# Kernel optimization log

Hardware: AMD Instinct MI355X
Metric: run time of the kernel (lower is better)

## Reference

```python
import jax, jax.numpy as jnp
import numpy as np

B, S, D = 2, 2048, 2048
H, HKV, HD = 32, 8, 64
G = H // HKV  # num_key_value_groups


def setup_inputs() -> dict:
    key = jax.random.key(0)
    ks = jax.random.split(key, 9)
    sc = 0.02
    return {
        "x": jax.random.normal(ks[0], (B, S, D), jnp.float32),
        "wq": jax.random.normal(ks[1], (H * HD, D), jnp.float32) * sc,
        "bq": jax.random.normal(ks[2], (H * HD,), jnp.float32) * sc,
        "wk": jax.random.normal(ks[3], (HKV * HD, D), jnp.float32) * sc,
        "bk": jax.random.normal(ks[4], (HKV * HD,), jnp.float32) * sc,
        "wv": jax.random.normal(ks[5], (HKV * HD, D), jnp.float32) * sc,
        "bv": jax.random.normal(ks[6], (HKV * HD,), jnp.float32) * sc,
        "wo": jax.random.normal(ks[7], (D, H * HD), jnp.float32) * sc,
        "bo": jax.random.normal(ks[8], (D,), jnp.float32) * sc,
    }


def reference(x, wq, bq, wk, bk, wv, bv, wo, bo):
    b, s, _ = x.shape
    # fused-QKV-style projections (nn.Linear: x @ W.T + b)
    q = (jnp.einsum("bsd,ed->bse", x, wq) + bq).reshape(b, s, H, HD)
    k = (jnp.einsum("bsd,ed->bse", x, wk) + bk).reshape(b, s, HKV, HD)
    v = (jnp.einsum("bsd,ed->bse", x, wv) + bv).reshape(b, s, HKV, HD)
    # (B, Hkv, G, S, hd): grouped query heads share a KV head — same math as
    # repeat_kv (expand+flatten) without materializing the expanded KV tensor
    q = q.transpose(0, 2, 1, 3).reshape(b, HKV, G, s, HD)
    k = k.transpose(0, 2, 1, 3)  # (B, Hkv, S, hd)
    v = v.transpose(0, 2, 1, 3)
    scale = 1.0 / jnp.sqrt(jnp.asarray(HD, x.dtype))
    scores = jnp.einsum("bkgqd,bktd->bkgqt", q, k) * scale  # (B,Hkv,G,S,S)
    causal = jnp.tril(jnp.ones((s, s), bool))
    scores = jnp.where(causal, scores, jnp.asarray(-jnp.inf, scores.dtype))
    probs = jax.nn.softmax(scores, axis=-1)
    o = jnp.einsum("bkgqt,bktd->bkgqd", probs, v)  # (B,Hkv,G,S,hd)
    o = o.reshape(b, H, s, HD).transpose(0, 2, 1, 3).reshape(b, s, H * HD)
    return jnp.einsum("bse,de->bsd", o, wo) + bo
```

## Files before the change

### kernel.cpp

```cpp
#include <hip/hip_runtime.h>
#include <hip/hip_bf16.h>
#include <cmath>

#define B_   2
#define S_   2048
#define D_   2048
#define H_   32
#define HKV_ 8
#define HD_  64

using bf16 = __hip_bfloat16;
typedef __bf16    bf16x8 __attribute__((ext_vector_type(8)));
typedef float     floatx4 __attribute__((ext_vector_type(4)));
typedef _Float16  half4 __attribute__((ext_vector_type(4)));
typedef _Float16  half8 __attribute__((ext_vector_type(8)));
typedef _Float16  half2v __attribute__((ext_vector_type(2)));

#if __has_builtin(__builtin_amdgcn_exp2f)
#define EXP2(x) __builtin_amdgcn_exp2f(x)
#else
#define EXP2(x) exp2f(x)
#endif

#define QSCALE 0.18033688011112042f

__device__ inline void async16(const void* g, void* l) {
  __builtin_amdgcn_global_load_lds(
      (const __attribute__((address_space(1))) void*)g,
      (__attribute__((address_space(3))) void*)l, 16, 0, 0);
}

__device__ inline half2v pkrtz(float a, float b) {
  return __builtin_bit_cast(half2v, __builtin_amdgcn_cvt_pkrtz(a, b));
}

#define MFMA32B(a, b, c) __builtin_amdgcn_mfma_f32_16x16x32_bf16((a), (b), (c), 0, 0, 0)
#define MFMA16H(a, b, c) __builtin_amdgcn_mfma_f32_16x16x16f16((a), (b), (c), 0, 0, 0)

__global__ void f2b_all(const float* __restrict__ x,  const float* __restrict__ wq,
                        const float* __restrict__ wk, const float* __restrict__ wv,
                        const float* __restrict__ wo,
                        bf16* __restrict__ xb,  bf16* __restrict__ wqb,
                        bf16* __restrict__ wkb, bf16* __restrict__ wvb,
                        bf16* __restrict__ wob) {
  const int i = blockIdx.x * blockDim.x + threadIdx.x;
  const float* src; bf16* dst; int off; float scale = 1.0f;
  if (i < 1048576)      { src = x;  dst = xb;  off = 0; }
  else if (i < 1572864) { src = wq; dst = wqb; off = 1048576; scale = QSCALE; }
  else if (i < 1703936) { src = wk; dst = wkb; off = 1572864; }
  else if (i < 1835008) { src = wv; dst = wvb; off = 1703936; }
  else                  { src = wo; dst = wob; off = 1835008; }
  const int j = i - off;
  float4 a  = ((const float4*)src)[2 * j];
  float4 b2 = ((const float4*)src)[2 * j + 1];
  alignas(16) bf16 t[8];
  t[0] = __float2bfloat16(a.x * scale);  t[1] = __float2bfloat16(a.y * scale);
  t[2] = __float2bfloat16(a.z * scale);  t[3] = __float2bfloat16(a.w * scale);
  t[4] = __float2bfloat16(b2.x * scale); t[5] = __float2bfloat16(b2.y * scale);
  t[6] = __float2bfloat16(b2.z * scale); t[7] = __float2bfloat16(b2.w * scale);
  ((uint4*)dst)[j] = *(const uint4*)t;
}

__device__ inline void gemm_body(const bf16* __restrict__ Ag, const bf16* __restrict__ Bg,
                                 const float* __restrict__ bias,
                                 float* __restrict__ C, int Ncol, int K, int bm, int colb,
                                 bf16* As, bf16* Bs) {
  const int tid  = threadIdx.x;
  const int wid  = tid >> 6, lane = tid & 63;
  const int lm   = lane & 15, quad = lane >> 4;
  const int wm   = (wid >> 1) * 64, wn = (wid & 1) * 64;

  floatx4 acc[4][4] = {};

  const int l0 = tid * 8;
  const int r0 = l0 >> 5, c0 = l0 & 31;
  const int r1 = r0 + 64;

  for (int k0 = 0; k0 < K; k0 += 32) {
    async16(Ag + (size_t)r0 * K + k0 + c0, &As[l0]);
    async16(Ag + (size_t)r1 * K + k0 + c0, &As[l0 + 2048]);
    async16(Bg + (size_t)r0 * K + k0 + c0, &Bs[l0]);
    async16(Bg + (size_t)r1 * K + k0 + c0, &Bs[l0 + 2048]);
    asm volatile("s_waitcnt vmcnt(0)" ::: "memory");
    __syncthreads();

    bf16x8 aF[4], bF[4];
#pragma unroll
    for (int mi = 0; mi < 4; ++mi)
      aF[mi] = *(const bf16x8*)&As[(wm + mi * 16 + lm) * 32 + quad * 8];
#pragma unroll
    for (int ni = 0; ni < 4; ++ni)
      bF[ni] = *(const bf16x8*)&Bs[(wn + ni * 16 + lm) * 32 + quad * 8];
#pragma unroll
    for (int mi = 0; mi < 4; ++mi)
#pragma unroll
      for (int ni = 0; ni < 4; ++ni)
        acc[mi][ni] = MFMA32B(bF[ni], aF[mi], acc[mi][ni]);
    __syncthreads();
  }

#pragma unroll
  for (int mi = 0; mi < 4; ++mi) {
    const int row = bm * 128 + wm + mi * 16 + lm;
#pragma unroll
    for (int ni = 0; ni < 4; ++ni) {
      const int col0 = colb + wn + ni * 16 + quad * 4;
      float4 bv4 = *(const float4*)&bias[col0];
      float4 o4;
      o4.x = acc[mi][ni][0] + bv4.x; o4.y = acc[mi][ni][1] + bv4.y;
      o4.z = acc[mi][ni][2] + bv4.z; o4.w = acc[mi][ni][3] + bv4.w;
      *(float4*)&C[(size_t)row * Ncol + col0] = o4;
    }
  }
}

__global__ __launch_bounds__(256, 2)
void gemm_o(const bf16* __restrict__ A, const bf16* __restrict__ Bm,
            const float* __restrict__ bias, float* __restrict__ C,
            int Ncol, int K) {
  __shared__ bf16 As[128 * 32];
  __shared__ bf16 Bs[128 * 32];
  const int bn = blockIdx.x, bm = blockIdx.y;
  gemm_body(A + (size_t)bm * 128 * K, Bm + (size_t)bn * 128 * K, bias,
            C, Ncol, K, bm, bn * 128, As, Bs);
}

__global__ __launch_bounds__(512, 2)
void gemm_qkv8(const bf16* __restrict__ xb, const bf16* __restrict__ Wcat,
               const float* __restrict__ bq, const float* __restrict__ bk,
               const float* __restrict__ bv,
               bf16* __restrict__ Qo, bf16* __restrict__ Ko,
               _Float16* __restrict__ VG) {
  constexpr int NT = D_ / 64;
  __shared__ bf16 L[65536];

  const int id = blockIdx.x;
  const int bn = id & 7;
  const int bm = id >> 3;

  const int tid = threadIdx.x;
  const int wid = tid >> 6, lane = tid & 63;
  const int lm = lane & 15, quad = lane >> 4;
  const int wm = wid >> 2, wn = wid & 3;

  const int cOff = (quad * 8) ^ (((lm >> 3) & 1) << 4);
  const bf16* LA0 = L + (wm * 64 + lm) * 32 + cOff;
  const bf16* LB0 = L + 8192 + (wn * 96 + lm) * 32 + cOff;

  const int r0 = tid >> 2;
  const int csrc = ((tid & 3) * 8) ^ (((tid >> 5) & 1) << 4);
  const bf16* Asrc = xb   + (size_t)(bm * 128 + r0) * D_ + csrc;
  const bf16* Bs0  = Wcat + (size_t)(bn * 384 + r0) * D_ + csrc;
  const bf16* Bs1  = Bs0 + (size_t)128 * D_;
  const bf16* Bs2  = Bs0 + (size_t)256 * D_;
  bf16* Ld = L + tid * 8;

  floatx4 acc[4][6] = {};

#define BARX() { asm volatile("" ::: "memory"); __builtin_amdgcn_s_barrier(); \
                 asm volatile("" ::: "memory"); }
#define LGKM0() asm volatile("s_waitcnt lgkmcnt(0)" ::: "memory")
#define STG_A(tt, hh, DB)  async16(Asrc + (tt) * 64 + (hh) * 32, (DB) + (hh) * 4096)
#define STG_B0(tt, hh, DB) async16(Bs0  + (tt) * 64 + (hh) * 32, (DB) + 8192 + (hh) * 12288)
#define STG_B1(tt, hh, DB) async16(Bs1  + (tt) * 64 + (hh) * 32, (DB) + 8192 + (hh) * 12288 + 4096)
#define STG_B2(tt, hh, DB) async16(Bs2  + (tt) * 64 + (hh) * 32, (DB) + 8192 + (hh) * 12288 + 8192)

  STG_A(0, 0, Ld); STG_B0(0, 0, Ld); STG_B1(0, 0, Ld); STG_B2(0, 0, Ld);
  STG_A(0, 1, Ld); STG_B0(0, 1, Ld); STG_B1(0, 1, Ld); STG_B2(0, 1, Ld);
  STG_A(1, 0, Ld + 32768); STG_B0(1, 0, Ld + 32768);
  STG_B1(1, 0, Ld + 32768); STG_B2(1, 0, Ld + 32768);
  asm volatile("s_waitcnt vmcnt(8)" ::: "memory");
  BARX();

  auto tile = [&](int t, const int BUF) __attribute__((always_inline)) {
    const bf16* LA = LA0 + BUF;
    const bf16* LB = LB0 + BUF;
    bf16* SD  = Ld + BUF;
    bf16* SDo = Ld + (BUF ^ 32768);
    const bool s1 = (t + 1) < NT, s2 = (t + 2) < NT;
    bf16x8 aF[4], bF[3];

#pragma unroll
    for (int i = 0; i < 4; ++i) aF[i] = *(const bf16x8*)(LA + i * 512);
#pragma unroll
    for (int i = 0; i < 3; ++i) bF[i] = *(const bf16x8*)(LB + i * 512);
    if (s1) { STG_A(t + 1, 1, SDo); STG_B0(t + 1, 1, SDo); }
    BARX(); LGKM0();
    __builtin_amdgcn_s_setprio(1);
#pragma unroll
    for (int mi = 0; mi < 4; ++mi)
#pragma unroll
      for (int ni = 0; ni < 3; ++ni)
        acc[mi][ni] = MFMA32B(bF[ni], aF[mi], acc[mi][ni]);
    __builtin_amdgcn_s_setprio(0);
    BARX();

#pragma unroll
    for (int i = 0; i < 3; ++i) bF[i] = *(const bf16x8*)(LB + (i + 3) * 512);
    if (s1) { STG_B1(t + 1, 1, SDo); STG_B2(t + 1, 1, SDo); }
    BARX(); LGKM0();
    __builtin_amdgcn_s_setprio(1);
#pragma unroll
    for (int mi = 0; mi < 4; ++mi)
#pragma unroll
      for (int ni = 0; ni < 3; ++ni)
        acc[mi][ni + 3] = MFMA32B(bF[ni], aF[mi], acc[mi][ni + 3]);
    __builtin_amdgcn_s_setprio(0);
    if (s1) { asm volatile("s_waitcnt vmcnt(8)" ::: "memory"); }
    else    { asm volatile("s_waitcnt vmcnt(0)" ::: "memory"); }
    BARX();

#pragma unroll
    for (int i = 0; i < 4; ++i) aF[i] = *(const bf16x8*)(LA + 4096 + i * 512);
#pragma unroll
    for (int i = 0; i < 3; ++i) bF[i] = *(const bf16x8*)(LB + 12288 + i * 512);
    if (s2) { STG_A(t + 2, 0, SD); STG_B0(t + 2, 0, SD); }
    BARX(); LGKM0();
    __builtin_amdgcn_s_setprio(1);
#pragma unroll
    for (int mi = 0; mi < 4; ++mi)
#pragma unroll
      for (int ni = 0; ni < 3; ++ni)
        acc[mi][ni] = MFMA32B(bF[ni], aF[mi], acc[mi][ni]);
    __builtin_amdgcn_s_setprio(0);
    BARX();

#pragma unroll
    for (int i = 0; i < 3; ++i) bF[i] = *(const bf16x8*)(LB + 12288 + (i + 3) * 512);
    if (s2) { STG_B1(t + 2, 0, SD); STG_B2(t + 2, 0, SD); }
    BARX(); LGKM0();
    __builtin_amdgcn_s_setprio(1);
#pragma unroll
    for (int mi = 0; mi < 4; ++mi)
#pragma unroll
      for (int ni = 0; ni < 3; ++ni)
        acc[mi][ni + 3] = MFMA32B(bF[ni], aF[mi], acc[mi][ni + 3]);
    __builtin_amdgcn_s_setprio(0);
    if (s2)      { asm volatile("s_waitcnt vmcnt(8)" ::: "memory"); }
    else if (s1) { asm volatile("s_waitcnt vmcnt(4)" ::: "memory"); }
    else         { asm volatile("s_waitcnt vmcnt(0)" ::: "memory"); }
    BARX();
  };

  for (int t = 0; t < NT; t += 2) { tile(t, 0); tile(t + 1, 32768); }

#undef BARX
#undef LGKM0
#undef STG_A
#undef STG_B0
#undef STG_B1
#undef STG_B2

#pragma unroll
  for (int mi = 0; mi < 4; ++mi) {
    const int row = bm * 128 + wm * 64 + mi * 16 + lm;
#pragma unroll
    for (int ni = 0; ni < 6; ++ni) {
      const int colf = bn * 384 + wn * 96 + ni * 16;
      const int col0 = colf + quad * 4;
      if (colf < 2048) {
        float4 bv4 = *(const float4*)&bq[col0];
        alignas(8) bf16 t4[4];
#pragma unroll
        for (int r = 0; r < 4; ++r)
          t4[r] = __float2bfloat16(acc[mi][ni][r] + ((const float*)&bv4)[r] * QSCALE);
        *(uint2*)&Qo[(size_t)row * (H_ * HD_) + col0] = *(const uint2*)t4;
      } else if (colf < 2560) {
        const int ck = col0 - 2048;
        float4 bv4 = *(const float4*)&bk[ck];
        alignas(8) bf16 t4[4];
#pragma unroll
        for (int r = 0; r < 4; ++r)
          t4[r] = __float2bfloat16(acc[mi][ni][r] + ((const float*)&bv4)[r]);
        *(uint2*)&Ko[(size_t)row * (HKV_ * HD_) + ck] = *(const uint2*)t4;
      } else {
        const int cv = col0 - 2560;
        const int kvh = cv >> 6, hd = cv & 63;
        const int nh = hd >> 4;
        const int bb = row >> 11, s2 = row & 2047;
        const int tl = s2 >> 6, kvin = s2 & 63;
        const int kc = kvin >> 4, qd = (kvin >> 2) & 3, j = kvin & 3;
        const size_t base = ((size_t)((bb * 8 + kvh) * 32 + tl) << 12) +
                            (size_t)(((kc * 2 + (nh >> 1)) * 4 + qd) * 128 +
                                     (nh & 1) * 4 + j);
        float4 bv4 = *(const float4*)&bv[cv];
#pragma unroll
        for (int r = 0; r < 4; ++r)
          VG[base + (size_t)(quad * 4 + r) * 8] =
              (_Float16)(acc[mi][ni][r] + ((const float*)&bv4)[r]);
      }
    }
  }
}

__global__ __launch_bounds__(256, 5)
void attn_kernel(const bf16* __restrict__ Q, const bf16* __restrict__ K,
                 const _Float16* __restrict__ VG, bf16* __restrict__ O) {
  const int tid = threadIdx.x;
  const int wid = tid >> 6, lane = tid & 63;
  const int lm = lane & 15, quad = lane >> 4;

  const int n   = blockIdx.y * 64 + blockIdx.x;
  const int x3  = n & 7, b1 = (n >> 3) & 1;
  const int pair = n >> 4;
  const int grp  = x3 * 2 + b1;
  const int b    = grp >> 3, kvh = grp & 7;
  const int head = kvh * 4 + wid;

  const int hi = 127 - pair, lo = pair;
  const int nt_hi = (hi >> 2) + 1;
  const int nt_lo = (lo >> 2) + 1;

  __shared__ bf16     Ks[2 * 64 * 64];
  __shared__ _Float16 Vs[2 * 64 * 64];

  const int tb[2] = {hi * 16, lo * 16};

  bf16x8 qf[2][2];
#pragma unroll
  for (int tt = 0; tt < 2; ++tt) {
    const size_t qg = ((size_t)(b * S_ + tb[tt] + lm)) * (H_ * HD_) + head * HD_;
#pragma unroll
    for (int kf = 0; kf < 2; ++kf)
      qf[tt][kf] = *(const bf16x8*)&Q[qg + kf * 32 + quad * 8];
  }

  half4 onesh;
#pragma unroll
  for (int j = 0; j < 4; ++j) onesh[j] = (_Float16)1.0f;

  floatx4 o_acc[2][4] = {};
  floatx4 lacc[2] = {};

  auto stage = [&](int t, int buf) {
    const int tr = tid >> 2;
    const int tc = (tid & 3) * 8;
#pragma unroll
    for (int c = 0; c < 2; ++c) {
      async16(&K[(size_t)(b * S_ + t * 64 + tr) * (HKV_ * HD_) + kvh * HD_ + c * 32 + tc],
              &Ks[buf * 4096 + c * 2048 + tid * 8]);
      async16(&VG[((size_t)(grp * 32 + t) << 12) + c * 2048 + tid * 8],
              &Vs[buf * 4096 + c * 2048 + tid * 8]);
    }
  };

  stage(0, 0);

  for (int t = 0; t < nt_hi; ++t) {
    const int cur = t & 1;
    asm volatile("s_waitcnt vmcnt(0)" ::: "memory");
    __syncthreads();
    if (t + 1 < nt_hi) stage(t + 1, cur ^ 1);

    const bf16*     Kb = &Ks[cur * 4096];
    const _Float16* Vb = &Vs[cur * 4096];
    const int t0 = t * 64;
    const int nact = (t < nt_lo) ? 2 : 1;

    int kcmax[2], kcross[2];
#pragma unroll
    for (int tt = 0; tt < 2; ++tt) {
      const int rel = tb[tt] + 15 - t0;
      kcmax[tt]  = (tt < nact) ? ((rel >> 4) >= 3 ? 4 : (rel >> 4) + 1) : 0;
      kcross[tt] = rel >> 4;
    }

    half4 ps[2] = {};

#pragma unroll
    for (int kc = 0; kc < 4; ++kc) {
      if (kc >= kcmax[0]) break;
      bf16x8 kb0 = *(const bf16x8*)&Kb[(kc * 16 + lm) * 32 + quad * 8];
      bf16x8 kb1 = *(const bf16x8*)&Kb[2048 + (kc * 16 + lm) * 32 + quad * 8];

      floatx4 sT[2];
      __builtin_amdgcn_s_setprio(1);
#pragma unroll
      for (int tt = 0; tt < 2; ++tt) {
        if (kc >= kcmax[tt]) continue;
        floatx4 s0 = {};
        s0 = MFMA32B(kb0, qf[tt][0], s0);
        sT[tt] = MFMA32B(kb1, qf[tt][1], s0);
      }
      __builtin_amdgcn_s_setprio(0);

      half8 v0 = *(const half8*)&Vb[(kc * 8 + quad) * 128 + lm * 8];
      half8 v1 = *(const half8*)&Vb[(kc * 8 + 4 + quad) * 128 + lm * 8];
      half4 v0l = __builtin_shufflevector(v0, v0, 0, 1, 2, 3);
      half4 v0h = __builtin_shufflevector(v0, v0, 4, 5, 6, 7);
      half4 v1l = __builtin_shufflevector(v1, v1, 0, 1, 2, 3);
      half4 v1h = __builtin_shufflevector(v1, v1, 4, 5, 6, 7);

      half4 pbk[2];
#pragma unroll
      for (int tt = 0; tt < 2; ++tt) {
        if (kc >= kcmax[tt]) continue;
        floatx4 s = sT[tt];
        if (kc == kcross[tt]) {
          const int qrel = tb[tt] + lm - t0;
#pragma unroll
          for (int r = 0; r < 4; ++r)
            if (kc * 16 + quad * 4 + r > qrel) s[r] = -__builtin_inff();
        }
        half2v c0 = pkrtz(EXP2(s[0]), EXP2(s[1]));
        half2v c1 = pkrtz(EXP2(s[2]), EXP2(s[3]));
        half4 pk = __builtin_shufflevector(c0, c1, 0, 1, 2, 3);
        pbk[tt] = pk;
        ps[tt] += pk;
      }

      __builtin_amdgcn_s_setprio(1);
#pragma unroll
      for (int tt = 0; tt < 2; ++tt) {
        if (kc >= kcmax[tt]) continue;
        o_acc[tt][0] = MFMA16H(v0l, pbk[tt], o_acc[tt][0]);
        o_acc[tt][1] = MFMA16H(v0h, pbk[tt], o_acc[tt][1]);
        o_acc[tt][2] = MFMA16H(v1l, pbk[tt], o_acc[tt][2]);
        o_acc[tt][3] = MFMA16H(v1h, pbk[tt], o_acc[tt][3]);
      }
      __builtin_amdgcn_s_setprio(0);
    }

#pragma unroll
    for (int tt = 0; tt < 2; ++tt)
      if (kcmax[tt]) lacc[tt] = MFMA16H(onesh, ps[tt], lacc[tt]);
  }

#pragma unroll
  for (int tt = 0; tt < 2; ++tt) {
    const float rl = 1.f / lacc[tt][0];
    const size_t rowg = (size_t)(b * S_ + tb[tt] + lm);
#pragma unroll
    for (int nh = 0; nh < 4; ++nh) {
      alignas(8) bf16 tmp[4];
#pragma unroll
      for (int r = 0; r < 4; ++r)
        tmp[r] = __float2bfloat16(o_acc[tt][nh][r] * rl);
      *(uint2*)&O[rowg * (H_ * HD_) + head * HD_ + nh * 16 + quad * 4] = *(uint2*)tmp;
    }
  }
}

extern "C" void kernel_launch(void* const* d_in, const int* in_sizes, int n_in,
                              void* d_out, int out_size, void* d_ws, size_t ws_size,
                              hipStream_t stream) {
  (void)in_sizes; (void)n_in; (void)out_size; (void)ws_size;
  const float* x  = (const float*)d_in[0];
  const float* wq = (const float*)d_in[1];
  const float* bq = (const float*)d_in[2];
  const float* wk = (const float*)d_in[3];
  const float* bk = (const float*)d_in[4];
  const float* wv = (const float*)d_in[5];
  const float* bv = (const float*)d_in[6];
  const float* wo = (const float*)d_in[7];
  const float* bo = (const float*)d_in[8];
  float* out = (float*)d_out;

  const int M = B_ * S_;
  const int E = H_ * HD_;
  const int EKV = HKV_ * HD_;

  char* ws = (char*)d_ws;
  size_t off = 0;
  auto alloc = [&](size_t bytes) {
    char* p = ws + off;
    off += (bytes + 255) & ~(size_t)255;
    return p;
  };
  bf16* xb   = (bf16*)alloc((size_t)M * D_ * 2);
  bf16* Wcat = (bf16*)alloc((size_t)(E + 2 * EKV) * D_ * 2);
  bf16* wob  = (bf16*)alloc((size_t)D_ * E * 2);
  bf16* Qb   = (bf16*)alloc((size_t)M * E * 2);
  bf16* Kb   = (bf16*)alloc((size_t)M * EKV * 2);
  _Float16* VG = (_Float16*)alloc((size_t)M * EKV * 2);
  bf16* Ob   = (bf16*)alloc((size_t)M * E * 2);

  bf16* wqb = Wcat;
  bf16* wkb = Wcat + (size_t)E * D_;
  bf16* wvb = Wcat + (size_t)(E + EKV) * D_;

  f2b_all<<<9216, 256, 0, stream>>>(x, wq, wk, wv, wo, xb, wqb, wkb, wvb, wob);

  gemm_qkv8<<<dim3(256), dim3(512), 0, stream>>>(xb, Wcat, bq, bk, bv,
                                                 Qb, Kb, VG);

  attn_kernel<<<dim3(64, 16), 256, 0, stream>>>(Qb, Kb, VG, Ob);

  gemm_o<<<dim3(D_ / 128, M / 128), 256, 0, stream>>>(Ob, wob, bo, out, D_, D_);
}
```

Baseline: 291.9 us.

## Replace output GEMM with pipelined 8-wave kernel; merge QKV half-steps

Replaces the simple single-buffered output-projection GEMM with a 512-thread kernel that uses a 128x256 tile, double-buffered async global-to-LDS loads with swizzled layout, and MFMA priority hints, so loads overlap with compute. The QKV GEMM inner step is also restructured: all six B fragments are loaded at once and the two half-phases (with their extra barriers) are merged into one. This cuts barrier and synchronisation overhead. In exchange it raises register pressure and issues all stage loads together, which could hurt occupancy or latency hiding.

```diff
diff --git a/kernel.cpp b/kernel.cpp
--- a/kernel.cpp
+++ b/kernel.cpp
@@ -36,6 +36,10 @@
 
 #define MFMA32B(a, b, c) __builtin_amdgcn_mfma_f32_16x16x32_bf16((a), (b), (c), 0, 0, 0)
 #define MFMA16H(a, b, c) __builtin_amdgcn_mfma_f32_16x16x16f16((a), (b), (c), 0, 0, 0)
+
+#define BARX() { asm volatile("" ::: "memory"); __builtin_amdgcn_s_barrier(); \
+                 asm volatile("" ::: "memory"); }
+#define LGKM0() asm volatile("s_waitcnt lgkmcnt(0)" ::: "memory")
 
 __global__ void f2b_all(const float* __restrict__ x,  const float* __restrict__ wq,
                         const float* __restrict__ wk, const float* __restrict__ wv,
@@ -61,70 +65,6 @@
   ((uint4*)dst)[j] = *(const uint4*)t;
 }
 
-__device__ inline void gemm_body(const bf16* __restrict__ Ag, const bf16* __restrict__ Bg,
-                                 const float* __restrict__ bias,
-                                 float* __restrict__ C, int Ncol, int K, int bm, int colb,
-                                 bf16* As, bf16* Bs) {
-  const int tid  = threadIdx.x;
-  const int wid  = tid >> 6, lane = tid & 63;
-  const int lm   = lane & 15, quad = lane >> 4;
-  const int wm   = (wid >> 1) * 64, wn = (wid & 1) * 64;
-
-  floatx4 acc[4][4] = {};
-
-  const int l0 = tid * 8;
-  const int r0 = l0 >> 5, c0 = l0 & 31;
-  const int r1 = r0 + 64;
-
-  for (int k0 = 0; k0 < K; k0 += 32) {
-    async16(Ag + (size_t)r0 * K + k0 + c0, &As[l0]);
-    async16(Ag + (size_t)r1 * K + k0 + c0, &As[l0 + 2048]);
-    async16(Bg + (size_t)r0 * K + k0 + c0, &Bs[l0]);
-    async16(Bg + (size_t)r1 * K + k0 + c0, &Bs[l0 + 2048]);
-    asm volatile("s_waitcnt vmcnt(0)" ::: "memory");
-    __syncthreads();
-
-    bf16x8 aF[4], bF[4];
-#pragma unroll
-    for (int mi = 0; mi < 4; ++mi)
-      aF[mi] = *(const bf16x8*)&As[(wm + mi * 16 + lm) * 32 + quad * 8];
-#pragma unroll
-    for (int ni = 0; ni < 4; ++ni)
-      bF[ni] = *(const bf16x8*)&Bs[(wn + ni * 16 + lm) * 32 + quad * 8];
-#pragma unroll
-    for (int mi = 0; mi < 4; ++mi)
-#pragma unroll
-      for (int ni = 0; ni < 4; ++ni)
-        acc[mi][ni] = MFMA32B(bF[ni], aF[mi], acc[mi][ni]);
-    __syncthreads();
-  }
-
-#pragma unroll
-  for (int mi = 0; mi < 4; ++mi) {
-    const int row = bm * 128 + wm + mi * 16 + lm;
-#pragma unroll
-    for (int ni = 0; ni < 4; ++ni) {
-      const int col0 = colb + wn + ni * 16 + quad * 4;
-      float4 bv4 = *(const float4*)&bias[col0];
-      float4 o4;
-      o4.x = acc[mi][ni][0] + bv4.x; o4.y = acc[mi][ni][1] + bv4.y;
-      o4.z = acc[mi][ni][2] + bv4.z; o4.w = acc[mi][ni][3] + bv4.w;
-      *(float4*)&C[(size_t)row * Ncol + col0] = o4;
-    }
-  }
-}
-
-__global__ __launch_bounds__(256, 2)
-void gemm_o(const bf16* __restrict__ A, const bf16* __restrict__ Bm,
-            const float* __restrict__ bias, float* __restrict__ C,
-            int Ncol, int K) {
-  __shared__ bf16 As[128 * 32];
-  __shared__ bf16 Bs[128 * 32];
-  const int bn = blockIdx.x, bm = blockIdx.y;
-  gemm_body(A + (size_t)bm * 128 * K, Bm + (size_t)bn * 128 * K, bias,
-            C, Ncol, K, bm, bn * 128, As, Bs);
-}
-
 __global__ __launch_bounds__(512, 2)
 void gemm_qkv8(const bf16* __restrict__ xb, const bf16* __restrict__ Wcat,
                const float* __restrict__ bq, const float* __restrict__ bk,
@@ -157,9 +97,6 @@
 
   floatx4 acc[4][6] = {};
 
-#define BARX() { asm volatile("" ::: "memory"); __builtin_amdgcn_s_barrier(); \
-                 asm volatile("" ::: "memory"); }
-#define LGKM0() asm volatile("s_waitcnt lgkmcnt(0)" ::: "memory")
 #define STG_A(tt, hh, DB)  async16(Asrc + (tt) * 64 + (hh) * 32, (DB) + (hh) * 4096)
 #define STG_B0(tt, hh, DB) async16(Bs0  + (tt) * 64 + (hh) * 32, (DB) + 8192 + (hh) * 12288)
 #define STG_B1(tt, hh, DB) async16(Bs1  + (tt) * 64 + (hh) * 32, (DB) + 8192 + (hh) * 12288 + 4096)
@@ -178,33 +115,21 @@
     bf16* SD  = Ld + BUF;
     bf16* SDo = Ld + (BUF ^ 32768);
     const bool s1 = (t + 1) < NT, s2 = (t + 2) < NT;
-    bf16x8 aF[4], bF[3];
+    bf16x8 aF[4], bF[6];
 
 #pragma unroll
     for (int i = 0; i < 4; ++i) aF[i] = *(const bf16x8*)(LA + i * 512);
 #pragma unroll
-    for (int i = 0; i < 3; ++i) bF[i] = *(const bf16x8*)(LB + i * 512);
-    if (s1) { STG_A(t + 1, 1, SDo); STG_B0(t + 1, 1, SDo); }
+    for (int i = 0; i < 6; ++i) bF[i] = *(const bf16x8*)(LB + i * 512);
+    if (s1) { STG_A(t + 1, 1, SDo); STG_B0(t + 1, 1, SDo);
+              STG_B1(t + 1, 1, SDo); STG_B2(t + 1, 1, SDo); }
     BARX(); LGKM0();
     __builtin_amdgcn_s_setprio(1);
 #pragma unroll
     for (int mi = 0; mi < 4; ++mi)
 #pragma unroll
-      for (int ni = 0; ni < 3; ++ni)
+      for (int ni = 0; ni < 6; ++ni)
         acc[mi][ni] = MFMA32B(bF[ni], aF[mi], acc[mi][ni]);
-    __builtin_amdgcn_s_setprio(0);
-    BARX();
-
-#pragma unroll
-    for (int i = 0; i < 3; ++i) bF[i] = *(const bf16x8*)(LB + (i + 3) * 512);
-    if (s1) { STG_B1(t + 1, 1, SDo); STG_B2(t + 1, 1, SDo); }
-    BARX(); LGKM0();
-    __builtin_amdgcn_s_setprio(1);
-#pragma unroll
-    for (int mi = 0; mi < 4; ++mi)
-#pragma unroll
-      for (int ni = 0; ni < 3; ++ni)
-        acc[mi][ni + 3] = MFMA32B(bF[ni], aF[mi], acc[mi][ni + 3]);
     __builtin_amdgcn_s_setprio(0);
     if (s1) { asm volatile("s_waitcnt vmcnt(8)" ::: "memory"); }
     else    { asm volatile("s_waitcnt vmcnt(0)" ::: "memory"); }
@@ -213,28 +138,16 @@
 #pragma unroll
     for (int i = 0; i < 4; ++i) aF[i] = *(const bf16x8*)(LA + 4096 + i * 512);
 #pragma unroll
-    for (int i = 0; i < 3; ++i) bF[i] = *(const bf16x8*)(LB + 12288 + i * 512);
-    if (s2) { STG_A(t + 2, 0, SD); STG_B0(t + 2, 0, SD); }
+    for (int i = 0; i < 6; ++i) bF[i] = *(const bf16x8*)(LB + 12288 + i * 512);
+    if (s2) { STG_A(t + 2, 0, SD); STG_B0(t + 2, 0, SD);
+              STG_B1(t + 2, 0, SD); STG_B2(t + 2, 0, SD); }
     BARX(); LGKM0();
     __builtin_amdgcn_s_setprio(1);
 #pragma unroll
     for (int mi = 0; mi < 4; ++mi)
 #pragma unroll
-      for (int ni = 0; ni < 3; ++ni)
+      for (int ni = 0; ni < 6; ++ni)
         acc[mi][ni] = MFMA32B(bF[ni], aF[mi], acc[mi][ni]);
-    __builtin_amdgcn_s_setprio(0);
-    BARX();
-
-#pragma unroll
-    for (int i = 0; i < 3; ++i) bF[i] = *(const bf16x8*)(LB + 12288 + (i + 3) * 512);
-    if (s2) { STG_B1(t + 2, 0, SD); STG_B2(t + 2, 0, SD); }
-    BARX(); LGKM0();
-    __builtin_amdgcn_s_setprio(1);
-#pragma unroll
-    for (int mi = 0; mi < 4; ++mi)
-#pragma unroll
-      for (int ni = 0; ni < 3; ++ni)
-        acc[mi][ni + 3] = MFMA32B(bF[ni], aF[mi], acc[mi][ni + 3]);
     __builtin_amdgcn_s_setprio(0);
     if (s2)      { asm volatile("s_waitcnt vmcnt(8)" ::: "memory"); }
     else if (s1) { asm volatile("s_waitcnt vmcnt(4)" ::: "memory"); }
@@ -244,8 +157,6 @@
 
   for (int t = 0; t < NT; t += 2) { tile(t, 0); tile(t + 1, 32768); }
 
-#undef BARX
-#undef LGKM0
 #undef STG_A
 #undef STG_B0
 #undef STG_B1
@@ -293,6 +204,110 @@
   }
 }
 
+__global__ __launch_bounds__(512, 2)
+void gemm_o8(const bf16* __restrict__ A, const bf16* __restrict__ Bm,
+             const float* __restrict__ bias, float* __restrict__ C) {
+  constexpr int NT = D_ / 64;
+  constexpr int BUFE = 24576;
+  __shared__ bf16 L[2 * BUFE];
+
+  const int id = blockIdx.x;
+  const int bn = id & 7;
+  const int bm = id >> 3;
+
+  const int tid = threadIdx.x;
+  const int wid = tid >> 6, lane = tid & 63;
+  const int lm = lane & 15, quad = lane >> 4;
+  const int wm = wid >> 2, wn = wid & 3;
+
+  const int cOff = (quad * 8) ^ (((lm >> 3) & 1) << 4);
+  const bf16* LA0 = L + (wm * 64 + lm) * 32 + cOff;
+  const bf16* LB0 = L + 4096 + (wn * 64 + lm) * 32 + cOff;
+
+  const int r0 = tid >> 2;
+  const int csrc = ((tid & 3) * 8) ^ (((tid >> 5) & 1) << 4);
+  const bf16* Asrc = A  + (size_t)(bm * 128 + r0) * D_ + csrc;
+  const bf16* Bs0  = Bm + (size_t)(bn * 256 + r0) * D_ + csrc;
+  const bf16* Bs1  = Bs0 + (size_t)128 * D_;
+  bf16* Ld = L + tid * 8;
+
+  floatx4 acc[4][4] = {};
+
+#define STG_A(tt, hh, DB)  async16(Asrc + (tt) * 64 + (hh) * 32, (DB) + (hh) * 12288)
+#define STG_B0(tt, hh, DB) async16(Bs0  + (tt) * 64 + (hh) * 32, (DB) + 4096 + (hh) * 12288)
+#define STG_B1(tt, hh, DB) async16(Bs1  + (tt) * 64 + (hh) * 32, (DB) + 8192 + (hh) * 12288)
+
+  STG_A(0, 0, Ld); STG_B0(0, 0, Ld); STG_B1(0, 0, Ld);
+  STG_A(0, 1, Ld); STG_B0(0, 1, Ld); STG_B1(0, 1, Ld);
+  STG_A(1, 0, Ld + BUFE); STG_B0(1, 0, Ld + BUFE); STG_B1(1, 0, Ld + BUFE);
+  asm volatile("s_waitcnt vmcnt(6)" ::: "memory");
+  BARX();
+
+  auto tile = [&](int t, const int BUF) __attribute__((always_inline)) {
+    const bf16* LA = LA0 + BUF;
+    const bf16* LB = LB0 + BUF;
+    bf16* SD  = Ld + BUF;
+    bf16* SDo = Ld + (BUF ^ BUFE);
+    const bool s1 = (t + 1) < NT, s2 = (t + 2) < NT;
+    bf16x8 aF[4], bF[4];
+
+#pragma unroll
+    for (int i = 0; i < 4; ++i) aF[i] = *(const bf16x8*)(LA + i * 512);
+#pragma unroll
+    for (int i = 0; i < 4; ++i) bF[i] = *(const bf16x8*)(LB + i * 512);
+    if (s1) { STG_A(t + 1, 1, SDo); STG_B0(t + 1, 1, SDo); STG_B1(t + 1, 1, SDo); }
+    BARX(); LGKM0();
+    __builtin_amdgcn_s_setprio(1);
+#pragma unroll
+    for (int mi = 0; mi < 4; ++mi)
+#pragma unroll
+      for (int ni = 0; ni < 4; ++ni)
+        acc[mi][ni] = MFMA32B(bF[ni], aF[mi], acc[mi][ni]);
+    __builtin_amdgcn_s_setprio(0);
+    if (s1) { asm volatile("s_waitcnt vmcnt(6)" ::: "memory"); }
+    else    { asm volatile("s_waitcnt vmcnt(0)" ::: "memory"); }
+    BARX();
+
+#pragma unroll
+    for (int i = 0; i < 4; ++i) aF[i] = *(const bf16x8*)(LA + 12288 + i * 512);
+#pragma unroll
+    for (int i = 0; i < 4; ++i) bF[i] = *(const bf16x8*)(LB + 12288 + i * 512);
+    if (s2) { STG_A(t + 2, 0, SD); STG_B0(t + 2, 0, SD); STG_B1(t + 2, 0, SD); }
+    BARX(); LGKM0();
+    __builtin_amdgcn_s_setprio(1);
+#pragma unroll
+    for (int mi = 0; mi < 4; ++mi)
+#pragma unroll
+      for (int ni = 0; ni < 4; ++ni)
+        acc[mi][ni] = MFMA32B(bF[ni], aF[mi], acc[mi][ni]);
+    __builtin_amdgcn_s_setprio(0);
+    if (s2)      { asm volatile("s_waitcnt vmcnt(6)" ::: "memory"); }
+    else if (s1) { asm volatile("s_waitcnt vmcnt(3)" ::: "memory"); }
+    else         { asm volatile("s_waitcnt vmcnt(0)" ::: "memory"); }
+    BARX();
+  };
+
+  for (int t = 0; t < NT; t += 2) { tile(t, 0); tile(t + 1, BUFE); }
+
+#undef STG_A
+#undef STG_B0
+#undef STG_B1
+
+#pragma unroll
+  for (int mi = 0; mi < 4; ++mi) {
+    const int row = bm * 128 + wm * 64 + mi * 16 + lm;
+#pragma unroll
+    for (int ni = 0; ni < 4; ++ni) {
+      const int col0 = bn * 256 + wn * 64 + ni * 16 + quad * 4;
+      float4 bv4 = *(const float4*)&bias[col0];
+      float4 o4;
+      o4.x = acc[mi][ni][0] + bv4.x; o4.y = acc[mi][ni][1] + bv4.y;
+      o4.z = acc[mi][ni][2] + bv4.z; o4.w = acc[mi][ni][3] + bv4.w;
+      *(float4*)&C[(size_t)row * D_ + col0] = o4;
+    }
+  }
+}
+
 __global__ __launch_bounds__(256, 5)
 void attn_kernel(const bf16* __restrict__ Q, const bf16* __restrict__ K,
                  const _Float16* __restrict__ VG, bf16* __restrict__ O) {
@@ -486,5 +501,5 @@
 
   attn_kernel<<<dim3(64, 16), 256, 0, stream>>>(Qb, Kb, VG, Ob);
 
-  gemm_o<<<dim3(D_ / 128, M / 128), 256, 0, stream>>>(Ob, wob, bo, out, D_, D_);
-}
+  gemm_o8<<<dim3(256), dim3(512), 0, stream>>>(Ob, wob, bo, out);
+}
```

Result: faster. 284.9 us (median of 2 runs) (-2.4%).
